# Performance work log

Measured on AMD Instinct MI355X. Metric: run time of the kernel, lower is better.

Reference implementation:

```python
import jax, jax.numpy as jnp
import numpy as np
from jax import lax

N, K, FEAT, HID = 50000, 16, 64, 128


def _linear(x, w, b=None):
    y = x @ w.T
    return y + b if b is not None else y


def _lstm_aggr(dense, wih, whh, bih, bhh):
    # dense: [N, K, F]; torch-style LSTM, return hidden state at last timestep
    n = dense.shape[0]
    hdim = whh.shape[1]
    h0 = jnp.zeros((n, hdim), dense.dtype)

    def step(carry, xt):
        h, c = carry
        gates = xt @ wih.T + bih + h @ whh.T + bhh
        i, f, g, o = jnp.split(gates, 4, axis=-1)
        c = jax.nn.sigmoid(f) * c + jax.nn.sigmoid(i) * jnp.tanh(g)
        h = jax.nn.sigmoid(o) * jnp.tanh(c)
        return (h, c), None

    (h, _), _ = lax.scan(step, (h0, h0), jnp.swapaxes(dense, 0, 1))
    return h


def _sage(x, src, dst, max_deg, pw, pb, wih, whh, bih, bhh, llw, llb, lrw):
    # PyG SAGEConv(aggr='lstm', project=True): project+relu source feats,
    # gather messages, pad per-dst neighbor sequences, LSTM-aggregate,
    # then lin_l(aggr) + lin_r(x_root). dst must be sorted (it is, by construction).
    n = x.shape[0]
    xp = jax.nn.relu(_linear(x, pw, pb))
    msgs = xp[src]                                      # [E, F]
    e = src.shape[0]
    counts = jax.ops.segment_sum(jnp.ones((e,), jnp.int32), dst, num_segments=n)
    offsets = jnp.concatenate([jnp.zeros((1,), jnp.int32), jnp.cumsum(counts)[:-1]])
    pos = jnp.arange(e, dtype=jnp.int32) - offsets[dst]  # slot within neighborhood
    dense = jnp.zeros((n, max_deg, xp.shape[1]), xp.dtype).at[dst, pos].set(msgs)
    aggr = _lstm_aggr(dense, wih, whh, bih, bhh)
    return _linear(aggr, llw, llb) + _linear(x, lrw)


def setup_inputs() -> dict:
    key = jax.random.key(0)
    ks = jax.random.split(key, 16)
    s = 0.05
    dst = jnp.repeat(jnp.arange(N, dtype=jnp.int32), K)  # sorted by destination, fixed degree K
    src = jax.random.randint(ks[0], (N * K,), 0, N, dtype=jnp.int32)
    return {
        "x": jax.random.normal(ks[1], (N, FEAT), jnp.float32),
        "edge_index": jnp.stack([src, dst]),
        "max_deg": K,
        "p1_proj_w": jax.random.normal(ks[2], (FEAT, FEAT)) * s,
        "p1_proj_b": jnp.zeros((FEAT,)),
        "p1_wih": jax.random.normal(ks[3], (4 * FEAT, FEAT)) * s,
        "p1_whh": jax.random.normal(ks[4], (4 * FEAT, FEAT)) * s,
        "p1_bih": jnp.zeros((4 * FEAT,)),
        "p1_bhh": jnp.zeros((4 * FEAT,)),
        "p1_ll_w": jax.random.normal(ks[5], (HID // 2, FEAT)) * s,
        "p1_ll_b": jnp.zeros((HID // 2,)),
        "p1_lr_w": jax.random.normal(ks[6], (HID // 2, FEAT)) * s,
        "p2_proj_w": jax.random.normal(ks[7], (HID // 2, HID // 2)) * s,
        "p2_proj_b": jnp.zeros((HID // 2,)),
        "p2_wih": jax.random.normal(ks[8], (4 * (HID // 2), HID // 2)) * s,
        "p2_whh": jax.random.normal(ks[9], (4 * (HID // 2), HID // 2)) * s,
        "p2_bih": jnp.zeros((4 * (HID // 2),)),
        "p2_bhh": jnp.zeros((4 * (HID // 2),)),
        "p2_ll_w": jax.random.normal(ks[10], (HID, HID // 2)) * s,
        "p2_ll_b": jnp.zeros((HID,)),
        "p2_lr_w": jax.random.normal(ks[11], (HID, HID // 2)) * s,
        "lin1_w": jax.random.normal(ks[12], (HID * 3 // 2, HID)) * s,
        "lin1_b": jnp.zeros((HID * 3 // 2,)),
        "lin2_w": jax.random.normal(ks[13], (HID // 2, HID * 3 // 2)) * s,
        "lin2_b": jnp.zeros((HID // 2,)),
        "lin3_w": jax.random.normal(ks[14], (HID // 2, HID // 2)) * s,
        "lin3_b": jnp.zeros((HID // 2,)),
    }


def reference(x, edge_index, max_deg,
              p1_proj_w, p1_proj_b, p1_wih, p1_whh, p1_bih, p1_bhh, p1_ll_w, p1_ll_b, p1_lr_w,
              p2_proj_w, p2_proj_b, p2_wih, p2_whh, p2_bih, p2_bhh, p2_ll_w, p2_ll_b, p2_lr_w,
              lin1_w, lin1_b, lin2_w, lin2_b, lin3_w, lin3_b):
    src, dst = edge_index[0], edge_index[1]
    h = jax.nn.relu(_sage(x, src, dst, max_deg, p1_proj_w, p1_proj_b, p1_wih, p1_whh, p1_bih, p1_bhh, p1_ll_w, p1_ll_b, p1_lr_w))
    h = jax.nn.relu(_sage(h, src, dst, max_deg, p2_proj_w, p2_proj_b, p2_wih, p2_whh, p2_bih, p2_bhh, p2_ll_w, p2_ll_b, p2_lr_w))
    h = jax.nn.relu(_linear(h, lin1_w, lin1_b))
    h = jax.nn.relu(_linear(h, lin2_w, lin2_b))
    h = jax.nn.relu(_linear(h, lin3_w, lin3_b))
    return (h, edge_index)
```

## Files before the change

kernel.cpp:

```cpp
#include <hip/hip_runtime.h>
#include <hip/hip_bf16.h>

typedef unsigned short u16;
typedef unsigned int u32;
typedef __attribute__((ext_vector_type(8))) short short8;
typedef __attribute__((ext_vector_type(4))) float f32x4;

#define KS1 1.44269504f
#define KS2 2.88539008f

__device__ __forceinline__ float bf2f(u16 u) {
    union { u32 i; float f; } v; v.i = ((u32)u) << 16; return v.f;
}
__device__ __forceinline__ u16 f2bf(float f) {
    union { float f; u32 i; } v; v.f = f;
    u32 r = v.i + 0x7fffu + ((v.i >> 16) & 1u);
    return (u16)(r >> 16);
}
__device__ __forceinline__ u32 pack_bf2(float lo, float hi) {
    return __builtin_amdgcn_perm(__float_as_uint(hi), __float_as_uint(lo), 0x07060302u);
}
__device__ __forceinline__ u32 pack_relu(float a, float b) {
    return (u32)f2bf(fmaxf(a, 0.f)) | ((u32)f2bf(fmaxf(b, 0.f)) << 16);
}
__device__ __forceinline__ f32x4 bias4(const u16* b) {
    uint2 u = *(const uint2*)b;
    f32x4 r;
    r[0] = bf2f((u16)(u.x & 0xffffu)); r[1] = bf2f((u16)(u.x >> 16));
    r[2] = bf2f((u16)(u.y & 0xffffu)); r[3] = bf2f((u16)(u.y >> 16));
    return r;
}
__device__ __forceinline__ void xwrite(u16* buf, int D2, int row, int quad, int jt, u32 w0, u32 w1) {
    int ch = jt * 2 + (quad >> 1);
    *(uint2*)(buf + row * D2 + ((ch ^ (row & 7)) << 3) + ((quad & 1) << 2)) = (uint2){w0, w1};
}
__device__ __forceinline__ short8 xread(const u16* buf, int D2, int row, int quad, int kc) {
    return *(const short8*)(buf + row * D2 + (((kc * 4 + quad) ^ (row & 7)) << 3));
}
#define MFMA16 __builtin_amdgcn_mfma_f32_16x16x32_bf16

__global__ __launch_bounds__(256) void k_pre(
    const u16* __restrict__ X, const u16* __restrict__ pw, const u16* __restrict__ pb,
    u16* __restrict__ XP, int M, int gb,
    const int* __restrict__ e, float* __restrict__ eout, int n4, int eb,
    const u16* __restrict__ w1i, const u16* __restrict__ w1h,
    const u16* __restrict__ w2i, const u16* __restrict__ w2h,
    u16* __restrict__ wss)
{
    const int bid = blockIdx.x;
    const int tid = threadIdx.x;
    if (bid >= gb + eb) {
        int mi = bid - gb - eb;
        const u16* Wsrc = (mi == 0) ? w1i : (mi == 1) ? w1h : (mi == 2) ? w2i : w2h;
        u16* Wdst = wss + (size_t)mi * 16384;
        for (int idx = tid; idx < 16384; idx += 256) {
            int row = idx >> 6;
            float sc = (row >= 128 && row < 192) ? KS2 : KS1;
            Wdst[idx] = f2bf(bf2f(Wsrc[idx]) * sc);
        }
        return;
    }
    if (bid >= gb) {
        int i = (bid - gb) * 256 + tid;
        if (i < n4) {
            int4 v = *(const int4*)(e + (size_t)i * 4);
            float4 o;
            o.x = (float)v.x; o.y = (float)v.y; o.z = (float)v.z; o.w = (float)v.w;
            *(float4*)(eout + (size_t)i * 4) = o;
        }
        return;
    }
    const int lane = tid & 63;
    const int wave = tid >> 6;
    const int row0 = (bid * 4 + wave) * 16;
    if (row0 >= M) return;
    const int col  = lane & 15;
    const int quad = lane >> 4;

    f32x4 c1[4];
#pragma unroll
    for (int jt = 0; jt < 4; ++jt) c1[jt] = (f32x4){0.f, 0.f, 0.f, 0.f};
    {
        const u16* xrow = X  + (size_t)(row0 + col) * 64 + quad * 8;
        const u16* wrow = pw + (size_t)col * 64 + quad * 8;
#pragma unroll
        for (int kc = 0; kc < 64; kc += 32) {
            short8 a = *(const short8*)(xrow + kc);
#pragma unroll
            for (int jt = 0; jt < 4; ++jt) {
                short8 b = *(const short8*)(wrow + (size_t)jt * 16 * 64 + kc);
                c1[jt] = MFMA16(a, b, c1[jt], 0, 0, 0);
            }
        }
    }
#pragma unroll
    for (int jt = 0; jt < 4; ++jt) {
        float bias = bf2f(pb[jt * 16 + col]);
#pragma unroll
        for (int r = 0; r < 4; ++r) {
            float v = fmaxf(c1[jt][r] + bias, 0.f);
            XP[(size_t)(row0 + quad * 4 + r) * 64 + jt * 16 + col] = f2bf(v);
        }
    }
}


#define NONLIN(ACC, CST, HW0, HW1)                                             \
    {                                                                          \
        float hv[4];                                                           \
        _Pragma("unroll") for (int r = 0; r < 4; ++r) {                        \
            float iv = ACC[0][r], fv = ACC[1][r], gv = ACC[2][r], ov = ACC[3][r]; \
            float e_i = __builtin_amdgcn_exp2f(-iv);                           \
            float e_f = __builtin_amdgcn_exp2f(-fv);                           \
            float e_g = __builtin_amdgcn_exp2f(gv);                            \
            float af  = 1.0f + e_f;                                            \
            float P   = (1.0f + e_i) * (1.0f + e_g);                           \
            float tt  = __builtin_fmaf(e_g, KS2, -KS2);                        \
            float num = __builtin_fmaf(tt, af, CST[r] * P);                    \
            float cn  = num * __builtin_amdgcn_rcpf(af * P);                   \
            CST[r] = cn;                                                       \
            float e_c = __builtin_amdgcn_exp2f(cn);                            \
            float e_o = __builtin_amdgcn_exp2f(-ov);                           \
            float roc = __builtin_amdgcn_rcpf((1.0f + e_o) * (1.0f + e_c));    \
            hv[r] = (e_c - 1.0f) * roc;                                        \
        }                                                                      \
        HW0 = pack_bf2(hv[0], hv[1]);                                          \
        HW1 = pack_bf2(hv[2], hv[3]);                                          \
    }

#define LSTM1_PROLOGUE                                                         \
    const int tid  = threadIdx.x;                                              \
    const int lane = tid & 63;                                                 \
    const int w    = tid >> 6;                                                 \
    const int col  = lane & 15;                                                \
    const int quad = lane >> 4;                                                \
    const int node0 = blockIdx.x * 16;                                         \
    if (node0 >= N) return;                                                    \
    const int nodeA = node0 + col;                                             \
    const bool act  = nodeA < N;                                               \
    const int ndA   = act ? nodeA : (N - 1);                                   \
    {                                                                          \
        int j = tid;                                                           \
        float sc = (j >= 128 && j < 192) ? KS2 : KS1;                          \
        lds_b[j] = (bf2f(bih[j]) + bf2f(bhh[j])) * sc;                         \
    }                                                                          \
    short8 wf[8], hf[8];                                                       \
    _Pragma("unroll") for (int g = 0; g < 4; ++g) {                            \
        int jt = w + 4 * g;                                                    \
        const u16* wi = wihs + (size_t)(jt * 16 + col) * 64 + quad * 8;        \
        const u16* wh = whhs + (size_t)(jt * 16 + col) * 64 + quad * 8;        \
        wf[g * 2 + 0] = *(const short8*)(wi);                                  \
        wf[g * 2 + 1] = *(const short8*)(wi + 32);                             \
        hf[g * 2 + 0] = *(const short8*)(wh);                                  \
        hf[g * 2 + 1] = *(const short8*)(wh + 32);                             \
    }                                                                          \
    int4 sidxA = *(const int4*)(src + (size_t)ndA * 16 + quad * 4);            \
    short8 xbA0, xbA1;                                                         \
    {                                                                          \
        int s = __shfl(sidxA.x, col, 64);                                      \
        const u16* p = xp + (size_t)s * 64 + quad * 8;                         \
        xbA0 = *(const short8*)p; xbA1 = *(const short8*)(p + 32);             \
    }

#define LSTM1_CORE_LOOP                                                        \
    short8 hbA0 = (short8){0,0,0,0,0,0,0,0};                                   \
    short8 hbA1 = hbA0;                                                        \
    float cA[4];                                                               \
    _Pragma("unroll") for (int i = 0; i < 4; ++i) cA[i] = 0.f;                 \
    __syncthreads();                                                           \
    _Pragma("unroll 1") for (int t = 0; t < 16; ++t) {                         \
        u16* hbuf = lds_h[t & 1];                                              \
        f32x4 acc[4];                                                          \
        _Pragma("unroll") for (int g = 0; g < 4; ++g) {                        \
            f32x4 bc = *(const f32x4*)(lds_b + (w + 4 * g) * 16 + quad * 4);   \
            acc[g] = MFMA16(wf[g * 2 + 0], xbA0, bc, 0, 0, 0);                 \
            acc[g] = MFMA16(wf[g * 2 + 1], xbA1, acc[g], 0, 0, 0);             \
        }                                                                      \
        short8 xn0 = xbA0, xn1 = xbA1;                                         \
        if (t < 15) {                                                          \
            int tn = t + 1;                                                    \
            int cv = (tn & 2) ? ((tn & 1) ? sidxA.w : sidxA.z)                 \
                              : ((tn & 1) ? sidxA.y : sidxA.x);                \
            int sn = __shfl(cv, ((tn >> 2) << 4) + col, 64);                   \
            const u16* p = xp + (size_t)sn * 64 + quad * 8;                    \
            xn0 = *(const short8*)p; xn1 = *(const short8*)(p + 32);           \
        }                                                                      \
        if (t > 0) {                                                           \
            _Pragma("unroll") for (int g = 0; g < 4; ++g) {                    \
                acc[g] = MFMA16(hf[g * 2 + 0], hbA0, acc[g], 0, 0, 0);         \
                acc[g] = MFMA16(hf[g * 2 + 1], hbA1, acc[g], 0, 0, 0);         \
            }                                                                  \
        }                                                                      \
        u32 hwA0, hwA1;                                                        \
        NONLIN(acc, cA, hwA0, hwA1)                                            \
        xwrite(hbuf, 64, col, quad, w, hwA0, hwA1);                            \
        __syncthreads();                                                       \
        hbA0 = xread(hbuf, 64, col, quad, 0);                                  \
        hbA1 = xread(hbuf, 64, col, quad, 1);                                  \
        xbA0 = xn0; xbA1 = xn1;                                                \
    }

__global__ __launch_bounds__(256, 4) void lstm_mid(
    const u16* __restrict__ xp, const int* __restrict__ src,
    const u16* __restrict__ wihs, const u16* __restrict__ whhs,
    const u16* __restrict__ bih, const u16* __restrict__ bhh,
    const u16* __restrict__ X,
    const u16* __restrict__ llw, const u16* __restrict__ llb,
    const u16* __restrict__ lrw,
    const u16* __restrict__ pw, const u16* __restrict__ pb,
    u16* __restrict__ Y1, u16* __restrict__ XP2, int N)
{
    __shared__ float lds_b[256];
    __shared__ u16 lds_h[2][16 * 64];
    __shared__ u16 bufY[16 * 64];

    LSTM1_PROLOGUE
    LSTM1_CORE_LOOP

    {
        const u16* wr  = llw + (size_t)(w * 16 + col) * 64 + quad * 8;
        short8 ll0 = *(const short8*)wr, ll1 = *(const short8*)(wr + 32);
        const u16* wr2 = lrw + (size_t)(w * 16 + col) * 64 + quad * 8;
        short8 lr0 = *(const short8*)wr2, lr1 = *(const short8*)(wr2 + 32);
        f32x4 bY = bias4(llb + w * 16 + quad * 4);

        const u16* xrA = X + (size_t)ndA * 64 + quad * 8;
        short8 rxA0 = *(const short8*)xrA, rxA1 = *(const short8*)(xrA + 32);

        f32x4 aA = MFMA16(ll0, hbA0, bY, 0, 0, 0);
        aA = MFMA16(ll1, hbA1, aA, 0, 0, 0);
        aA = MFMA16(lr0, rxA0, aA, 0, 0, 0);
        aA = MFMA16(lr1, rxA1, aA, 0, 0, 0);

        u32 yA0 = pack_relu(aA[0], aA[1]), yA1 = pack_relu(aA[2], aA[3]);
        if (act) *(uint2*)(Y1 + (size_t)nodeA * 64 + w * 16 + quad * 4) = (uint2){yA0, yA1};
        xwrite(bufY, 64, col, quad, w, yA0, yA1);
        __syncthreads();

        const u16* wp = pw + (size_t)(w * 16 + col) * 64 + quad * 8;
        short8 p0 = *(const short8*)wp, p1 = *(const short8*)(wp + 32);
        f32x4 bp = bias4(pb + w * 16 + quad * 4);

        short8 ybA0 = xread(bufY, 64, col, quad, 0);
        short8 ybA1 = xread(bufY, 64, col, quad, 1);

        f32x4 a2A = MFMA16(p0, ybA0, bp, 0, 0, 0);
        a2A = MFMA16(p1, ybA1, a2A, 0, 0, 0);

        if (act) *(uint2*)(XP2 + (size_t)nodeA * 64 + w * 16 + quad * 4) =
            (uint2){pack_relu(a2A[0], a2A[1]), pack_relu(a2A[2], a2A[3])};
    }
}

__global__ __launch_bounds__(256, 4) void lstm_post(
    const u16* __restrict__ xp, const int* __restrict__ src,
    const u16* __restrict__ wihs, const u16* __restrict__ whhs,
    const u16* __restrict__ bih, const u16* __restrict__ bhh,
    const u16* __restrict__ Y1,
    const u16* __restrict__ llw2, const u16* __restrict__ llb2,
    const u16* __restrict__ lrw2,
    const u16* __restrict__ w1m, const u16* __restrict__ b1m,
    const u16* __restrict__ w2m, const u16* __restrict__ b2m,
    const u16* __restrict__ w3m, const u16* __restrict__ b3m,
    float* __restrict__ outp, int N)
{
    __shared__ float lds_b[256];
    __shared__ u16 lds_h[2][16 * 64];
    __shared__ u16 bufA[16 * 128];
    __shared__ u16 bufB[16 * 192];

    LSTM1_PROLOGUE
    LSTM1_CORE_LOOP

    {
        const u16* yrA = Y1 + (size_t)ndA * 64 + quad * 8;
        short8 ryA0 = *(const short8*)yrA, ryA1 = *(const short8*)(yrA + 32);

#pragma unroll
        for (int ti = 0; ti < 2; ++ti) {
            int jt = 2 * w + ti;
            const u16* wr = llw2 + (size_t)(jt * 16 + col) * 64 + quad * 8;
            short8 l0 = *(const short8*)wr, l1 = *(const short8*)(wr + 32);
            const u16* wr2 = lrw2 + (size_t)(jt * 16 + col) * 64 + quad * 8;
            short8 r0 = *(const short8*)wr2, r1 = *(const short8*)(wr2 + 32);
            f32x4 b0 = bias4(llb2 + jt * 16 + quad * 4);
            f32x4 aA = MFMA16(l0, hbA0, b0, 0, 0, 0);
            aA = MFMA16(l1, hbA1, aA, 0, 0, 0);
            aA = MFMA16(r0, ryA0, aA, 0, 0, 0);
            aA = MFMA16(r1, ryA1, aA, 0, 0, 0);
            xwrite(bufA, 128, col, quad, jt, pack_relu(aA[0], aA[1]), pack_relu(aA[2], aA[3]));
        }
        __syncthreads();

        short8 y2A[4];
#pragma unroll
        for (int kc = 0; kc < 4; ++kc) y2A[kc] = xread(bufA, 128, col, quad, kc);

#pragma unroll
        for (int ti = 0; ti < 3; ++ti) {
            int jt = 3 * w + ti;
            const u16* wr = w1m + (size_t)(jt * 16 + col) * 128 + quad * 8;
            short8 wk[4];
#pragma unroll
            for (int kc = 0; kc < 4; ++kc) wk[kc] = *(const short8*)(wr + kc * 32);
            f32x4 b1v = bias4(b1m + jt * 16 + quad * 4);
            f32x4 aA = b1v;
#pragma unroll
            for (int kc = 0; kc < 4; ++kc) aA = MFMA16(wk[kc], y2A[kc], aA, 0, 0, 0);
            xwrite(bufB, 192, col, quad, jt, pack_relu(aA[0], aA[1]), pack_relu(aA[2], aA[3]));
        }
        __syncthreads();

        short8 t1A[6];
#pragma unroll
        for (int kc = 0; kc < 6; ++kc) t1A[kc] = xread(bufB, 192, col, quad, kc);

        {
            const u16* wr = w2m + (size_t)(w * 16 + col) * 192 + quad * 8;
            f32x4 b2v = bias4(b2m + w * 16 + quad * 4);
            f32x4 aA = b2v;
#pragma unroll
            for (int kc = 0; kc < 6; ++kc) {
                short8 wk = *(const short8*)(wr + kc * 32);
                aA = MFMA16(wk, t1A[kc], aA, 0, 0, 0);
            }
            xwrite(bufA, 64, col, quad, w, pack_relu(aA[0], aA[1]), pack_relu(aA[2], aA[3]));
        }
        __syncthreads();

        short8 t2A0 = xread(bufA, 64, col, quad, 0);
        short8 t2A1 = xread(bufA, 64, col, quad, 1);
        {
            const u16* wr = w3m + (size_t)(w * 16 + col) * 64 + quad * 8;
            short8 l0 = *(const short8*)wr, l1 = *(const short8*)(wr + 32);
            f32x4 b3v = bias4(b3m + w * 16 + quad * 4);
            f32x4 aA = MFMA16(l0, t2A0, b3v, 0, 0, 0);
            aA = MFMA16(l1, t2A1, aA, 0, 0, 0);
            if (act) {
                float4 oA;
                oA.x = fmaxf(aA[0], 0.f); oA.y = fmaxf(aA[1], 0.f);
                oA.z = fmaxf(aA[2], 0.f); oA.w = fmaxf(aA[3], 0.f);
                *(float4*)(outp + (size_t)nodeA * 64 + w * 16 + quad * 4) = oA;
            }
        }
    }
}

extern "C" void kernel_launch(void* const* d_in, const int* in_sizes, int n_in,
                              void* d_out, int out_size, void* d_ws, size_t ws_size,
                              hipStream_t stream)
{
    const u16* x       = (const u16*)d_in[0];
    const int* edge    = (const int*)d_in[1];
    const u16* p1_pw   = (const u16*)d_in[3];
    const u16* p1_pb   = (const u16*)d_in[4];
    const u16* p1_wih  = (const u16*)d_in[5];
    const u16* p1_whh  = (const u16*)d_in[6];
    const u16* p1_bih  = (const u16*)d_in[7];
    const u16* p1_bhh  = (const u16*)d_in[8];
    const u16* p1_llw  = (const u16*)d_in[9];
    const u16* p1_llb  = (const u16*)d_in[10];
    const u16* p1_lrw  = (const u16*)d_in[11];
    const u16* p2_pw   = (const u16*)d_in[12];
    const u16* p2_pb   = (const u16*)d_in[13];
    const u16* p2_wih  = (const u16*)d_in[14];
    const u16* p2_whh  = (const u16*)d_in[15];
    const u16* p2_bih  = (const u16*)d_in[16];
    const u16* p2_bhh  = (const u16*)d_in[17];
    const u16* p2_llw  = (const u16*)d_in[18];
    const u16* p2_llb  = (const u16*)d_in[19];
    const u16* p2_lrw  = (const u16*)d_in[20];
    const u16* lin1w   = (const u16*)d_in[21];
    const u16* lin1b   = (const u16*)d_in[22];
    const u16* lin2w   = (const u16*)d_in[23];
    const u16* lin2b   = (const u16*)d_in[24];
    const u16* lin3w   = (const u16*)d_in[25];
    const u16* lin3b   = (const u16*)d_in[26];
    (void)n_in; (void)ws_size;

    const int N  = in_sizes[0] / 64;
    const int E2 = in_sizes[1];
    const int* srcIdx = edge;

    char* w = (char*)d_ws;
    u16* wss   = (u16*)(w);
    u16* xp1   = (u16*)(w + 1u  * 1024 * 1024);
    u16* xp2   = (u16*)(w + 8u  * 1024 * 1024);
    u16* bufY1 = (u16*)(w + 15u * 1024 * 1024);
    u16* wih1s = wss;
    u16* whh1s = wss + 16384;
    u16* wih2s = wss + 32768;
    u16* whh2s = wss + 49152;

    float* out_h    = (float*)d_out;
    float* out_edge = (float*)d_out + (size_t)N * 64;
    (void)out_size;

    const int gb  = (N + 63) / 64;
    const int gbl = (N + 15) / 16;
    const int n4 = E2 / 4;
    const int eb = (n4 + 255) / 256;

    dim3 block(256);

    hipLaunchKernelGGL(k_pre, dim3(gb + eb + 4), block, 0, stream,
                       x, p1_pw, p1_pb, xp1, N, gb,
                       edge, out_edge, n4, eb,
                       p1_wih, p1_whh, p2_wih, p2_whh, wss);
    hipLaunchKernelGGL(lstm_mid, dim3(gbl), block, 0, stream,
                       xp1, srcIdx, wih1s, whh1s, p1_bih, p1_bhh,
                       x, p1_llw, p1_llb, p1_lrw, p2_pw, p2_pb, bufY1, xp2, N);
    hipLaunchKernelGGL(lstm_post, dim3(gbl), block, 0, stream,
                       xp2, srcIdx, wih2s, whh2s, p2_bih, p2_bhh,
                       bufY1, p2_llw, p2_llb, p2_lrw,
                       lin1w, lin1b, lin2w, lin2b, lin3w, lin3b, out_h, N);
}
```

Measured before the change: 341.9 us.

## Prefetch all neighbor feature rows into swizzled LDS before LSTM loop

The prologue now gathers all 16 timesteps of neighbor feature rows for the 16-node block into a 32KB XOR-swizzled shared buffer, with the loads issued in batches of four. The recurrent loop then reads its per-step inputs from LDS instead of doing a dependent global gather each step. This moves gather latency off the sequential recurrence. In exchange it adds a large up-front load phase and extra LDS per block, which may reduce occupancy. The epilogue scratch buffers now alias the new LDS region.

```diff
diff --git a/kernel.cpp b/kernel.cpp
--- a/kernel.cpp
+++ b/kernel.cpp
@@ -128,7 +128,7 @@
         HW1 = pack_bf2(hv[2], hv[3]);                                          \
     }
 
-#define LSTM1_PROLOGUE                                                         \
+#define LSTMS_PROLOGUE                                                         \
     const int tid  = threadIdx.x;                                              \
     const int lane = tid & 63;                                                 \
     const int w    = tid >> 6;                                                 \
@@ -144,6 +144,30 @@
         float sc = (j >= 128 && j < 192) ? KS2 : KS1;                          \
         lds_b[j] = (bf2f(bih[j]) + bf2f(bhh[j])) * sc;                         \
     }                                                                          \
+    {                                                                          \
+        const int rr   = lane >> 3;                  \
+        const int ch   = lane & 7;                   \
+        const int slot = ch ^ rr;                    \
+        _Pragma("unroll") for (int half = 0; half < 2; ++half) {               \
+            int sik[4];                                                        \
+            _Pragma("unroll") for (int k = 0; k < 4; ++k) {                    \
+                int kk = half * 4 + k;                                         \
+                int t  = w * 4 + (kk >> 1);                                    \
+                int r  = (kk & 1) * 8 + rr;                                    \
+                int nrow = node0 + r; if (nrow >= N) nrow = N - 1;             \
+                sik[k] = src[nrow * 16 + t];                                   \
+            }                                                                  \
+            short8 vk[4];                                                      \
+            _Pragma("unroll") for (int k = 0; k < 4; ++k)                      \
+                vk[k] = *(const short8*)(xp + (size_t)sik[k] * 64 + ch * 8);   \
+            _Pragma("unroll") for (int k = 0; k < 4; ++k) {                    \
+                int kk = half * 4 + k;                                         \
+                int t  = w * 4 + (kk >> 1);                                    \
+                int r  = (kk & 1) * 8 + rr;                                    \
+                *(short8*)(xs + t * 1024 + r * 64 + slot * 8) = vk[k];         \
+            }                                                                  \
+        }                                                                      \
+    }                                                                          \
     short8 wf[8], hf[8];                                                       \
     _Pragma("unroll") for (int g = 0; g < 4; ++g) {                            \
         int jt = w + 4 * g;                                                    \
@@ -154,20 +178,20 @@
         hf[g * 2 + 0] = *(const short8*)(wh);                                  \
         hf[g * 2 + 1] = *(const short8*)(wh + 32);                             \
     }                                                                          \
-    int4 sidxA = *(const int4*)(src + (size_t)ndA * 16 + quad * 4);            \
+    __syncthreads();                                                           \
+    const int q0 = quad ^ (col & 7);                                           \
     short8 xbA0, xbA1;                                                         \
     {                                                                          \
-        int s = __shfl(sidxA.x, col, 64);                                      \
-        const u16* p = xp + (size_t)s * 64 + quad * 8;                         \
-        xbA0 = *(const short8*)p; xbA1 = *(const short8*)(p + 32);             \
-    }
-
-#define LSTM1_CORE_LOOP                                                        \
+        const u16* p = xs + col * 64;                                          \
+        xbA0 = *(const short8*)(p + q0 * 8);                                   \
+        xbA1 = *(const short8*)(p + (q0 ^ 4) * 8);                             \
+    }
+
+#define LSTMS_CORE_LOOP                                                        \
     short8 hbA0 = (short8){0,0,0,0,0,0,0,0};                                   \
     short8 hbA1 = hbA0;                                                        \
     float cA[4];                                                               \
     _Pragma("unroll") for (int i = 0; i < 4; ++i) cA[i] = 0.f;                 \
-    __syncthreads();                                                           \
     _Pragma("unroll 1") for (int t = 0; t < 16; ++t) {                         \
         u16* hbuf = lds_h[t & 1];                                              \
         f32x4 acc[4];                                                          \
@@ -178,12 +202,9 @@
         }                                                                      \
         short8 xn0 = xbA0, xn1 = xbA1;                                         \
         if (t < 15) {                                                          \
-            int tn = t + 1;                                                    \
-            int cv = (tn & 2) ? ((tn & 1) ? sidxA.w : sidxA.z)                 \
-                              : ((tn & 1) ? sidxA.y : sidxA.x);                \
-            int sn = __shfl(cv, ((tn >> 2) << 4) + col, 64);                   \
-            const u16* p = xp + (size_t)sn * 64 + quad * 8;                    \
-            xn0 = *(const short8*)p; xn1 = *(const short8*)(p + 32);           \
+            const u16* p = xs + (t + 1) * 1024 + col * 64;                     \
+            xn0 = *(const short8*)(p + q0 * 8);                                \
+            xn1 = *(const short8*)(p + (q0 ^ 4) * 8);                          \
         }                                                                      \
         if (t > 0) {                                                           \
             _Pragma("unroll") for (int g = 0; g < 4; ++g) {                    \
@@ -210,12 +231,13 @@
     const u16* __restrict__ pw, const u16* __restrict__ pb,
     u16* __restrict__ Y1, u16* __restrict__ XP2, int N)
 {
+    __shared__ u16 xs[16 * 1024];
     __shared__ float lds_b[256];
     __shared__ u16 lds_h[2][16 * 64];
-    __shared__ u16 bufY[16 * 64];
-
-    LSTM1_PROLOGUE
-    LSTM1_CORE_LOOP
+    u16* bufY = xs;
+
+    LSTMS_PROLOGUE
+    LSTMS_CORE_LOOP
 
     {
         const u16* wr  = llw + (size_t)(w * 16 + col) * 64 + quad * 8;
@@ -264,13 +286,14 @@
     const u16* __restrict__ w3m, const u16* __restrict__ b3m,
     float* __restrict__ outp, int N)
 {
+    __shared__ u16 xs[16 * 1024];
     __shared__ float lds_b[256];
     __shared__ u16 lds_h[2][16 * 64];
-    __shared__ u16 bufA[16 * 128];
-    __shared__ u16 bufB[16 * 192];
-
-    LSTM1_PROLOGUE
-    LSTM1_CORE_LOOP
+    u16* bufA = xs;
+    u16* bufB = xs + 2048;
+
+    LSTMS_PROLOGUE
+    LSTMS_CORE_LOOP
 
     {
         const u16* yrA = Y1 + (size_t)ndA * 64 + quad * 8;
```

Result: faster. 279.5 us (-18.3%).
